# Performance work log

Measured on AMD Instinct MI355X. Metric: run time of the kernel, lower is better.

Reference implementation:

```python
import jax, jax.numpy as jnp
import numpy as np

RADIUS = 0.1
NSAMPLE = 64
NEVENT = 2048
B, N, D = 4, 16384, 62
CHANNEL = D + 2  # 64


def index_events(events, idx):
    # events: [B, N, C], idx: [B, ...] -> [B, ..., C]
    return jax.vmap(lambda e, i: e[i])(events, idx)


def square_distance(src, dst):
    # src: [B, S, 2], dst: [B, N, 2] -> [B, S, N]
    return (jnp.sum(src ** 2, -1)[:, :, None]
            + jnp.sum(dst ** 2, -1)[:, None, :]
            - 2.0 * jnp.einsum('bsc,bnc->bsn', src, dst))


def research_circle(radius, nsample, xy, new_xy):
    n = xy.shape[1]
    sqrdists = square_distance(new_xy, xy)            # [B, S, N]
    ar = jnp.arange(n, dtype=jnp.int32)
    group_idx = jnp.where(sqrdists > radius ** 2, n, ar)  # out-of-ball -> N (sorts last)
    group_idx = jnp.sort(group_idx, axis=-1)[:, :, :nsample]
    first = group_idx[:, :, :1]
    return jnp.where(group_idx == n, first, group_idx)     # [B, S, nsample]


def reference(xy, events, fps_idx, affine_alpha, affine_beta):
    b, _, c = xy.shape
    new_xy = index_events(xy, fps_idx)                     # [B, S, 2]
    idx = research_circle(RADIUS, NSAMPLE, xy, new_xy)     # [B, S, K]
    grouped_xy = index_events(xy, idx)                     # [B, S, K, 2]
    grouped_events = index_events(events, idx)             # [B, S, K, D]
    # Normalize (normalize='center')
    g = jnp.concatenate([grouped_events, grouped_xy], axis=-1)  # [B, S, K, D+2]
    mean = jnp.mean(g, axis=2, keepdims=True)              # [B, S, 1, C]
    centered = g - mean
    std = jnp.std(centered.reshape(b, -1), axis=-1, ddof=1)[:, None, None, None]
    g = centered / (std + 1e-05)
    new_events = affine_alpha * g + affine_beta            # [B, S, K, 64]
    return new_xy, new_events


def setup_inputs() -> dict:
    key = jax.random.key(0)
    k1, k2, k3 = jax.random.split(key, 3)
    xy = jax.random.uniform(k1, (B, N, 2), dtype=jnp.float32)
    events = jax.random.normal(k2, (B, N, D), dtype=jnp.float32)
    fps_idx = jax.random.randint(k3, (B, NEVENT), 0, N, dtype=jnp.int32)
    affine_alpha = jnp.ones((1, 1, 1, CHANNEL), dtype=jnp.float32)
    affine_beta = jnp.zeros((1, 1, 1, CHANNEL), dtype=jnp.float32)
    return {"xy": xy, "events": events, "fps_idx": fps_idx,
            "affine_alpha": affine_alpha, "affine_beta": affine_beta}
```

## Files before the change

### kernel.cpp

```cpp
#include <hip/hip_runtime.h>
#include <stdint.h>
#include <math.h>

#define NPTS 16384
#define DEV 62
#define NEVENT 2048
#define NSAMPLE 64
#define CH 64
#define NBATCH 4
#define STOT (NBATCH * NEVENT)
#define M_PER_BATCH (NEVENT * NSAMPLE * CH)

#define OUT1_BASE 16384
#define REG_STRIDE (NSAMPLE * CH)
#define SL_MEAN 64
#define SL_INV 128
#define SL_SS 129

__global__ __launch_bounds__(256) void knn_kernel(
    const float2* __restrict__ xy,
    const int* __restrict__ fps,
    float* __restrict__ out)
{
    int wave = blockIdx.x * 4 + (threadIdx.x >> 6);
    int lane = threadIdx.x & 63;
    int b = wave >> 11;

    const float2* xyb = xy + b * NPTS;
    int qi = fps[wave];
    float2 q = xyb[qi];
    if (lane == 0) ((float2*)out)[wave] = q;

    float ssq = __fadd_rn(__fmul_rn(q.x, q.x), __fmul_rn(q.y, q.y));
    const float thr = 0.01f;

    int* regidx = (int*)(out + OUT1_BASE + (size_t)wave * REG_STRIDE);
    int m = 0;
    int first = -1;

    for (int base = 0; base < NPTS; base += 64) {
        float2 p = xyb[base + lane];
        float ssp = __fadd_rn(__fmul_rn(p.x, p.x), __fmul_rn(p.y, p.y));
        float dot = __builtin_fmaf(q.y, p.y, __fmul_rn(q.x, p.x));
        float d   = __fsub_rn(__fadd_rn(ssq, ssp), __fmul_rn(2.0f, dot));
        bool ok = !(d > thr);
        unsigned long long bal = __ballot(ok);
        if (first < 0 && bal != 0ull)
            first = base + (__ffsll((unsigned long long)bal) - 1);
        if (ok) {
            int pos = m + __popcll(bal & ((1ull << lane) - 1ull));
            if (pos < NSAMPLE) regidx[pos] = base + lane;
        }
        m += __popcll(bal);
        if (m >= NSAMPLE) break;
    }
    if (m < NSAMPLE) {
        for (int p = m + lane; p < NSAMPLE; p += 64)
            regidx[p] = first;
    }
}

__global__ __launch_bounds__(256) void stats_kernel(
    const float2* __restrict__ xy,
    const float* __restrict__ ev,
    float* __restrict__ out)
{
    int s = blockIdx.x;
    int b = s >> 11;
    int tid = threadIdx.x;
    float* reg = out + OUT1_BASE + (size_t)s * REG_STRIDE;

    __shared__ int sidx[NSAMPLE];
    __shared__ float ssum[2][256];
    __shared__ float smean[CH];
    __shared__ float swred[4];

    if (tid < NSAMPLE) sidx[tid] = ((const int*)reg)[tid];
    __syncthreads();

    int c2 = tid & 31;
    int kq = tid >> 5;

    const float* evb = ev + (size_t)b * NPTS * DEV;
    const float2* xyb = xy + b * NPTS;

    float g0[8], g1[8];
    float a0 = 0.f, a1 = 0.f;
#pragma unroll
    for (int j = 0; j < 8; ++j) {
        int row = sidx[8 * j + kq];
        float2 v;
        if (c2 < 31) v = *(const float2*)(evb + (size_t)row * DEV + 2 * c2);
        else         v = xyb[row];
        g0[j] = v.x; g1[j] = v.y;
        a0 += v.x;   a1 += v.y;
    }
    ssum[0][tid] = a0;
    ssum[1][tid] = a1;
    __syncthreads();

    if (tid < CH) {
        int which = tid >> 5, cc = tid & 31;
        float t = 0.f;
#pragma unroll
        for (int q = 0; q < 8; ++q) t += ssum[which][q * 32 + cc];
        smean[2 * cc + which] = t * (1.0f / NSAMPLE);
    }
    __syncthreads();

    if (tid < CH) reg[SL_MEAN + tid] = smean[tid];

    float m0 = smean[2 * c2], m1 = smean[2 * c2 + 1];
    float ss = 0.f;
#pragma unroll
    for (int j = 0; j < 8; ++j) {
        float c0 = g0[j] - m0;
        float c1 = g1[j] - m1;
        ss += c0 * c0 + c1 * c1;
    }

    for (int off = 32; off > 0; off >>= 1) ss += __shfl_down(ss, off, 64);
    if ((tid & 63) == 0) swred[tid >> 6] = ss;
    __syncthreads();
    if (tid == 0) reg[SL_SS] = swred[0] + swred[1] + swred[2] + swred[3];
}

__global__ __launch_bounds__(256) void reduce_std_kernel(float* __restrict__ out)
{
    int b = blockIdx.x;
    int tid = threadIdx.x;
    double acc = 0.0;
    for (int i = tid; i < NEVENT; i += 256)
        acc += (double)out[OUT1_BASE + (size_t)(b * NEVENT + i) * REG_STRIDE + SL_SS];
    __shared__ double sd[256];
    __shared__ float sinv;
    sd[tid] = acc;
    __syncthreads();
    for (int off = 128; off > 0; off >>= 1) {
        if (tid < off) sd[tid] += sd[tid + off];
        __syncthreads();
    }
    if (tid == 0) {
        double stdv = sqrt(sd[0] / (double)(M_PER_BATCH - 1));
        sinv = (float)(1.0 / (stdv + 1e-5));
    }
    __syncthreads();
    float inv = sinv;
    for (int i = tid; i < NEVENT; i += 256)
        out[OUT1_BASE + (size_t)(b * NEVENT + i) * REG_STRIDE + SL_INV] = inv;
}

__global__ __launch_bounds__(256) void finalize_kernel(
    const float2* __restrict__ xy,
    const float* __restrict__ ev,
    const float* __restrict__ alpha,
    const float* __restrict__ beta,
    float* __restrict__ out)
{
    int s = blockIdx.x;
    int b = s >> 11;
    int tid = threadIdx.x;
    float* reg = out + OUT1_BASE + (size_t)s * REG_STRIDE;

    __shared__ int sidx[NSAMPLE];
    __shared__ float sm[CH], sa[CH], sbet[CH];
    __shared__ float sinv;

    if (tid < NSAMPLE) {
        sidx[tid] = ((const int*)reg)[tid];
        sm[tid] = reg[SL_MEAN + tid];
    } else if (tid < 128) {
        sa[tid - 64] = alpha[tid - 64];
        sbet[tid - 64] = beta[tid - 64];
    } else if (tid == 128) {
        sinv = reg[SL_INV];
    }
    __syncthreads();

    int c2 = tid & 31;
    int kq = tid >> 5;
    float inv = sinv;

    const float* evb = ev + (size_t)b * NPTS * DEV;
    const float2* xyb = xy + b * NPTS;

    float m0 = sm[2 * c2],   m1 = sm[2 * c2 + 1];
    float al0 = sa[2 * c2],  al1 = sa[2 * c2 + 1];
    float be0 = sbet[2 * c2], be1 = sbet[2 * c2 + 1];

    float2* outp = (float2*)reg;
#pragma unroll
    for (int j = 0; j < 8; ++j) {
        int row = sidx[8 * j + kq];
        float2 v;
        if (c2 < 31) v = *(const float2*)(evb + (size_t)row * DEV + 2 * c2);
        else         v = xyb[row];
        float2 r;
        r.x = al0 * ((v.x - m0) * inv) + be0;
        r.y = al1 * ((v.y - m1) * inv) + be1;
        outp[256 * j + tid] = r;
    }
}

extern "C" void kernel_launch(void* const* d_in, const int* in_sizes, int n_in,
                              void* d_out, int out_size, void* d_ws, size_t ws_size,
                              hipStream_t stream) {
    const float2* xy    = (const float2*)d_in[0];
    const float*  ev    = (const float*)d_in[1];
    const int*    fps   = (const int*)d_in[2];
    const float*  alpha = (const float*)d_in[3];
    const float*  beta  = (const float*)d_in[4];
    float* out = (float*)d_out;
    (void)d_ws; (void)ws_size;

    knn_kernel<<<STOT / 4, 256, 0, stream>>>(xy, fps, out);
    stats_kernel<<<STOT, 256, 0, stream>>>(xy, ev, out);
    reduce_std_kernel<<<NBATCH, 256, 0, stream>>>(out);
    finalize_kernel<<<STOT, 256, 0, stream>>>(xy, ev, alpha, beta, out);
}
```

Before: 209.9 us.

## Swizzle block-to-query mapping across XCDs and batch KNN scan loads by four

Adds block index swizzles so that consecutive block IDs, which are dealt round-robin across the eight XCDs, map to queries from the same batch within each XCD. The aim is better per-XCD L2 locality for the xy and events gathers in the knn, stats and finalize kernels. The KNN scan now issues four coalesced point loads per iteration before processing them, which raises memory-level parallelism. In exchange, up to 192 extra points may be scanned past the early-exit point.

```diff
diff --git a/kernel.cpp b/kernel.cpp
--- a/kernel.cpp
+++ b/kernel.cpp
@@ -17,12 +17,24 @@
 #define SL_INV 128
 #define SL_SS 129
 
+__device__ __forceinline__ int swz_query8192(int blk) {
+    int x = blk & 7;
+    int j = blk >> 3;
+    return (x & 3) * NEVENT + (x >> 2) * (NEVENT / 2) + j;
+}
+__device__ __forceinline__ int swz_group2048(int blk) {
+    int x = blk & 7;
+    int j = blk >> 3;
+    return (x & 3) * (NEVENT / 4) + (x >> 2) * (NEVENT / 8) + j;
+}
+
 __global__ __launch_bounds__(256) void knn_kernel(
     const float2* __restrict__ xy,
     const int* __restrict__ fps,
     float* __restrict__ out)
 {
-    int wave = blockIdx.x * 4 + (threadIdx.x >> 6);
+    int grp  = swz_group2048(blockIdx.x);
+    int wave = grp * 4 + (threadIdx.x >> 6);
     int lane = threadIdx.x & 63;
     int b = wave >> 11;
 
@@ -38,20 +50,30 @@
     int m = 0;
     int first = -1;
 
-    for (int base = 0; base < NPTS; base += 64) {
-        float2 p = xyb[base + lane];
-        float ssp = __fadd_rn(__fmul_rn(p.x, p.x), __fmul_rn(p.y, p.y));
-        float dot = __builtin_fmaf(q.y, p.y, __fmul_rn(q.x, p.x));
-        float d   = __fsub_rn(__fadd_rn(ssq, ssp), __fmul_rn(2.0f, dot));
-        bool ok = !(d > thr);
-        unsigned long long bal = __ballot(ok);
-        if (first < 0 && bal != 0ull)
-            first = base + (__ffsll((unsigned long long)bal) - 1);
-        if (ok) {
-            int pos = m + __popcll(bal & ((1ull << lane) - 1ull));
-            if (pos < NSAMPLE) regidx[pos] = base + lane;
-        }
-        m += __popcll(bal);
+    for (int base = 0; base < NPTS; base += 256) {
+        float2 p0 = xyb[base       + lane];
+        float2 p1 = xyb[base +  64 + lane];
+        float2 p2 = xyb[base + 128 + lane];
+        float2 p3 = xyb[base + 192 + lane];
+
+        auto proc = [&](float2 p, int idxbase) {
+            float ssp = __fadd_rn(__fmul_rn(p.x, p.x), __fmul_rn(p.y, p.y));
+            float dot = __builtin_fmaf(q.y, p.y, __fmul_rn(q.x, p.x));
+            float d   = __fsub_rn(__fadd_rn(ssq, ssp), __fmul_rn(2.0f, dot));
+            bool ok = !(d > thr);
+            unsigned long long bal = __ballot(ok);
+            if (first < 0 && bal != 0ull)
+                first = idxbase + (__ffsll((unsigned long long)bal) - 1);
+            if (ok) {
+                int pos = m + __popcll(bal & ((1ull << lane) - 1ull));
+                if (pos < NSAMPLE) regidx[pos] = idxbase + lane;
+            }
+            m += __popcll(bal);
+        };
+        proc(p0, base);
+        proc(p1, base + 64);
+        proc(p2, base + 128);
+        proc(p3, base + 192);
         if (m >= NSAMPLE) break;
     }
     if (m < NSAMPLE) {
@@ -65,7 +87,7 @@
     const float* __restrict__ ev,
     float* __restrict__ out)
 {
-    int s = blockIdx.x;
+    int s = swz_query8192(blockIdx.x);
     int b = s >> 11;
     int tid = threadIdx.x;
     float* reg = out + OUT1_BASE + (size_t)s * REG_STRIDE;
@@ -157,7 +179,7 @@
     const float* __restrict__ beta,
     float* __restrict__ out)
 {
-    int s = blockIdx.x;
+    int s = swz_query8192(blockIdx.x);
     int b = s >> 11;
     int tid = threadIdx.x;
     float* reg = out + OUT1_BASE + (size_t)s * REG_STRIDE;
```

Result: faster. 195.4 us (-6.9%).
